# Kernel optimization log

Measured on AMD Instinct MI355X. Metric: run time of the kernel, lower is better.

Reference implementation:

```python
import jax, jax.numpy as jnp
import numpy as np

BH, TQ, TK, DK = 64, 1024, 1024, 64  # B_h = B*H = 4*16


def setup_inputs() -> dict:
    key = jax.random.key(0)
    kq, kk, kv, km = jax.random.split(key, 4)
    Q = jax.random.normal(kq, (BH, TQ, DK), dtype=jnp.float32)
    K = jax.random.normal(kk, (BH, TK, DK), dtype=jnp.float32)
    V = jax.random.normal(kv, (BH, TK, DK), dtype=jnp.float32)
    mask = jax.random.randint(km, (BH, TK), 0, 2).astype(bool)  # 2D padding mask
    return {"Q": Q, "K": K, "V": V, "mask": mask, "head_ablation": 3, "num_heads": 16}


def reference(Q, K, V, mask, head_ablation, num_heads):
    B_h, T_q, d_k = Q.shape
    T_k = K.shape[1]
    # scores = Q K^T / sqrt(d_k), full [B_h, T_q, T_k] matrix as in the original
    scores = jnp.einsum('bqd,bkd->bqk', Q, K) / jnp.sqrt(jnp.asarray(d_k, Q.dtype))
    # 2D mask -> broadcast over query dim (mask.unsqueeze(1).expand in torch)
    m = jnp.broadcast_to(mask[:, None, :], (B_h, T_q, T_k))
    scores = jnp.where(m, scores, jnp.finfo(scores.dtype).min)
    weights = jax.nn.softmax(scores, axis=-1)
    # zero rows whose mask is fully off (torch fully_masked branch)
    fully_masked = m.sum(axis=-1, keepdims=True) == 0
    weights = jnp.where(fully_masked, jnp.zeros((), weights.dtype), weights)
    # head ablation: zero attention weights of one head
    B = B_h // num_heads
    weights = (weights.reshape(B, num_heads, T_q, T_k)
                      .at[:, head_ablation].set(0.0)
                      .reshape(B_h, T_q, T_k))
    # dropout_p = 0.0 -> identity
    output = jnp.einsum('bqk,bkd->bqd', weights, V)
    return (output, weights)
```

## Files before the change

kernel.cpp:

```cpp
#include <hip/hip_runtime.h>
#include <hip/hip_bf16.h>
#include <cfloat>
#include <cstdint>

#define BH 64
#define TQ 1024
#define TK 1024
#define DK 64
#define WSTR 1032

typedef __attribute__((ext_vector_type(8))) short short8;
typedef __attribute__((ext_vector_type(4))) short short4v;
typedef __attribute__((ext_vector_type(4))) float f32x4;

__device__ __forceinline__ short bf16r(float f) {
    union { float f; unsigned u; } x; x.f = f;
    unsigned r = x.u + 0x7fffu + ((x.u >> 16) & 1u);
    return (short)(r >> 16);
}

__device__ __forceinline__ float bf2f(short s) {
    union { unsigned u; float f; } x; x.u = ((unsigned)(unsigned short)s) << 16;
    return x.f;
}

__device__ __forceinline__ short8 load8_bf16_nt(const float* p) {
    f32x4 a = __builtin_nontemporal_load((const f32x4*)p);
    f32x4 b = __builtin_nontemporal_load((const f32x4*)(p + 4));
    short8 r;
    r[0] = bf16r(a[0]); r[1] = bf16r(a[1]); r[2] = bf16r(a[2]); r[3] = bf16r(a[3]);
    r[4] = bf16r(b[0]); r[5] = bf16r(b[1]); r[6] = bf16r(b[2]); r[7] = bf16r(b[3]);
    return r;
}

__device__ __forceinline__ short8 load8_bf16(const float* p) {
    f32x4 a = *(const f32x4*)p;
    f32x4 b = *(const f32x4*)(p + 4);
    short8 r;
    r[0] = bf16r(a[0]); r[1] = bf16r(a[1]); r[2] = bf16r(a[2]); r[3] = bf16r(a[3]);
    r[4] = bf16r(b[0]); r[5] = bf16r(b[1]); r[6] = bf16r(b[2]); r[7] = bf16r(b[3]);
    return r;
}

__global__ __launch_bounds__(256) void pack_kv(const float* __restrict__ K,
                                               const float* __restrict__ V,
                                               const void* __restrict__ mask,
                                               short* __restrict__ Kp,
                                               short* __restrict__ Vp,
                                               float* __restrict__ Mf) {
    __shared__ short tile[64 * 72];
    __shared__ int mflags[2];
    const int tid = threadIdx.x;
    const int bid = blockIdx.x;

    if (bid < 2048) {
        const int g = bid * 256 + tid;
        const int lane = g & 63, half = (g >> 6) & 1, tg = (g >> 7) & 63, b = g >> 13;
        const int key = tg * 16 + (lane & 15);
        const int d = half * 32 + (lane >> 4) * 8;
        short8 o = load8_bf16_nt(K + ((size_t)b * TK + key) * DK + d);
        *(short8*)(Kp + (size_t)g * 8) = o;
    } else if (bid < 3072) {
        const int vb = bid - 2048;
        const int k0 = (vb & 15) * 64, b = vb >> 4;
        #pragma unroll
        for (int it = 0; it < 4; ++it) {
            int lin = it * 256 + tid;
            int kl = lin >> 4;
            int d0 = (lin & 15) * 4;
            f32x4 v = __builtin_nontemporal_load(
                (const f32x4*)(V + ((size_t)b * TK + k0 + kl) * DK + d0));
            short4v o; o[0] = bf16r(v[0]); o[1] = bf16r(v[1]); o[2] = bf16r(v[2]); o[3] = bf16r(v[3]);
            *(short4v*)&tile[kl * 72 + d0] = o;
        }
        __syncthreads();
        #pragma unroll
        for (int it = 0; it < 4; ++it) {
            int lin = it * 256 + tid;
            int d = lin & 63;
            int kg = (lin >> 6) * 4;
            int key = k0 + kg;
            int kk = key >> 5;
            int quad = (kg >> 3) & 3, j0 = kg & 7;
            int lane = (d & 15) + 16 * quad, t = d >> 4;
            short4v o;
            #pragma unroll
            for (int i = 0; i < 4; ++i) o[i] = tile[(kg + i) * 72 + d];
            *(short4v*)&Vp[((((size_t)b * 32 + kk) * 4 + t) * 512) + lane * 8 + j0] = o;
        }
    } else {
        const int b = bid - 3072;
        if (tid == 0) { mflags[0] = 0; mflags[1] = 0; }
        __syncthreads();
        {
            unsigned v = ((const unsigned*)mask)[tid];
            bool f32pat = (v == 0x3f800000u);
            bool u8pat = (v > 1u) && !f32pat;
            unsigned long long bu = __ballot(u8pat);
            unsigned long long bf = __ballot(f32pat);
            if ((tid & 63) == 0) {
                if (bu) atomicOr(&mflags[0], 1);
                if (bf) atomicOr(&mflags[1], 1);
            }
        }
        __syncthreads();
        const int mode = mflags[0] ? 0 : (mflags[1] ? 2 : 1);
        const uint8_t* m8  = (const uint8_t*)mask + (size_t)b * TK;
        const int*     m32 = (const int*)mask     + (size_t)b * TK;
        const float*   mfp = (const float*)mask   + (size_t)b * TK;
        #pragma unroll
        for (int i = 0; i < 4; ++i) {
            int col = i * 256 + tid;
            bool mk = (mode == 0) ? (m8[col] != 0)
                    : (mode == 1) ? (m32[col] != 0)
                                  : (mfp[col] != 0.0f);
            Mf[(size_t)b * TK + col] = mk ? 1.0f : 0.0f;
        }
    }
}

__global__ __launch_bounds__(256, 4) void attn_fused(const float* __restrict__ Q,
                                                     const short* __restrict__ Kp,
                                                     const short* __restrict__ Vp,
                                                     const float* __restrict__ Mf,
                                                     float* __restrict__ Wout,
                                                     float* __restrict__ O,
                                                     const int* __restrict__ ha_p,
                                                     const int* __restrict__ nh_p) {
    __shared__ short Wlds[16 * WSTR];
    __shared__ float red2[16][4];

    const int tid = threadIdx.x;
    const int id = blockIdx.x;
    const int b = (id & 7) + ((id >> 7) & 7) * 8;
    const int qt = (id >> 3) & 15;
    const int q0 = qt * 64;

    if ((b % nh_p[0]) == ha_p[0]) {
        const f32x4 z = {0.f, 0.f, 0.f, 0.f};
        #pragma unroll 4
        for (int i = 0; i < 64; ++i)
            __builtin_nontemporal_store(z, (f32x4*)&Wout[((size_t)b * TQ + q0 + i) * TK + tid * 4]);
        #pragma unroll
        for (int i = 0; i < 4; ++i)
            __builtin_nontemporal_store(z,
                (f32x4*)&O[((size_t)b * TQ + q0 + i * 16 + (tid >> 4)) * DK + (tid & 15) * 4]);
        return;
    }

    const int lane = tid & 63, wave = tid >> 6;
    const int m = lane & 15, quad = lane >> 4;
    const int kw = wave * 256;

    const float* mfp = Mf + (size_t)b * TK + kw;
    const short* kpb = Kp + ((size_t)b * 64 + wave * 16) * 1024 + lane * 8;
    const short* vpb = Vp + (((size_t)b * 32) * 4 + wave) * 512 + lane * 8;

    for (int sub = 0; sub < 4; ++sub) {
        const int qs = q0 + sub * 16;

        const float* qrow = Q + ((size_t)b * TQ + qs + m) * DK + quad * 8;
        short8 a0 = load8_bf16(qrow);
        short8 a1 = load8_bf16(qrow + 32);

        float sum = 0.f;
        #pragma unroll 4
        for (int t = 0; t < 16; ++t) {
            short8 k0 = *(const short8*)(kpb + t * 1024);
            short8 k1 = *(const short8*)(kpb + t * 1024 + 512);
            f32x4 c = {0.f, 0.f, 0.f, 0.f};
            c = __builtin_amdgcn_mfma_f32_16x16x32_bf16(k0, a0, c, 0, 0, 0);
            c = __builtin_amdgcn_mfma_f32_16x16x32_bf16(k1, a1, c, 0, 0, 0);
            float4 mf = *(const float4*)(mfp + t * 16 + quad * 4);
            short4v pw;
            #pragma unroll
            for (int r = 0; r < 4; ++r) {
                float p = ((const float*)&mf)[r] * __expf(fminf(c[r] * 0.125f, 60.f));
                sum += p;
                pw[r] = bf16r(p);
            }
            *(short4v*)&Wlds[m * WSTR + kw + t * 16 + quad * 4] = pw;
        }
        sum += __shfl_xor(sum, 16);
        sum += __shfl_xor(sum, 32);
        if (quad == 0) red2[m][wave] = sum;
        __syncthreads();

        #pragma unroll 4
        for (int i = 0; i < 16; ++i) {
            float4 s4 = *(float4*)red2[i];
            float tot = (s4.x + s4.y) + (s4.z + s4.w);
            float inv = (tot == 0.f) ? 0.f : 1.0f / tot;
            short4v p4 = *(short4v*)&Wlds[i * WSTR + tid * 4];
            f32x4 w;
            w[0] = bf2f(p4[0]) * inv; w[1] = bf2f(p4[1]) * inv;
            w[2] = bf2f(p4[2]) * inv; w[3] = bf2f(p4[3]) * inv;
            __builtin_nontemporal_store(w, (f32x4*)&Wout[((size_t)b * TQ + qs + i) * TK + tid * 4]);
        }

        float inv4[4];
        #pragma unroll
        for (int r = 0; r < 4; ++r) {
            float4 s4 = *(float4*)red2[quad * 4 + r];
            float tot = (s4.x + s4.y) + (s4.z + s4.w);
            inv4[r] = (tot == 0.f) ? 0.f : 1.0f / tot;
        }
        f32x4 oacc = {0.f, 0.f, 0.f, 0.f};
        #pragma unroll 8
        for (int kk = 0; kk < 32; ++kk) {
            short8 a = *(const short8*)&Wlds[m * WSTR + kk * 32 + quad * 8];
            short8 bb = *(const short8*)(vpb + (size_t)kk * 2048);
            oacc = __builtin_amdgcn_mfma_f32_16x16x32_bf16(a, bb, oacc, 0, 0, 0);
        }
        #pragma unroll
        for (int r = 0; r < 4; ++r)
            __builtin_nontemporal_store(oacc[r] * inv4[r],
                &O[((size_t)b * TQ + qs + quad * 4 + r) * DK + wave * 16 + m]);

        __syncthreads();
    }
}

extern "C" void kernel_launch(void* const* d_in, const int* in_sizes, int n_in,
                              void* d_out, int out_size, void* d_ws, size_t ws_size,
                              hipStream_t stream) {
    const float* Q    = (const float*)d_in[0];
    const float* Kmat = (const float*)d_in[1];
    const float* V    = (const float*)d_in[2];
    const void*  mask = d_in[3];
    const int*   ha   = (const int*)d_in[4];
    const int*   nh   = (const int*)d_in[5];

    float* out     = (float*)d_out;
    float* weights = out + (size_t)BH * TQ * DK;

    short* Kp = (short*)d_ws;
    short* Vp = Kp + (size_t)BH * TK * DK;
    float* Mf = (float*)(Vp + (size_t)BH * TK * DK);

    pack_kv<<<dim3(3136), 256, 0, stream>>>(Kmat, V, mask, Kp, Vp, Mf);
    attn_fused<<<dim3(TQ / 64 * BH), 256, 0, stream>>>(Q, Kp, Vp, Mf, weights, out, ha, nh);
}
```

Measured before the change: 357.7 us.

## Fold score scale into K packing, prefetch Q, split PV accumulators

Several micro-optimizations land together. The 1/sqrt(dk) scale is folded into the K bf16 packing, and the fminf clamp is dropped from the exp. The next Q sub-tile is prefetched during the normalization phase. Softmax sums use four independent accumulators, and bf16 packing uses the hardware pair conversion. The PV MFMA chain is split into two accumulators to break the dependency. Dropping the clamp risks overflow if a score exceeds the exp range, and scaling before bf16 rounding slightly changes numerics.

```diff
diff --git a/kernel.cpp b/kernel.cpp
--- a/kernel.cpp
+++ b/kernel.cpp
@@ -24,12 +24,18 @@
     return x.f;
 }
 
-__device__ __forceinline__ short8 load8_bf16_nt(const float* p) {
+__device__ __forceinline__ unsigned pk_bf16(float a, float b) {
+    union { __hip_bfloat162 h; unsigned u; } r;
+    r.h = __float22bfloat162_rn(make_float2(a, b));
+    return r.u;
+}
+
+__device__ __forceinline__ short8 load8_bf16_nt_s(const float* p, float s) {
     f32x4 a = __builtin_nontemporal_load((const f32x4*)p);
     f32x4 b = __builtin_nontemporal_load((const f32x4*)(p + 4));
     short8 r;
-    r[0] = bf16r(a[0]); r[1] = bf16r(a[1]); r[2] = bf16r(a[2]); r[3] = bf16r(a[3]);
-    r[4] = bf16r(b[0]); r[5] = bf16r(b[1]); r[6] = bf16r(b[2]); r[7] = bf16r(b[3]);
+    r[0] = bf16r(a[0] * s); r[1] = bf16r(a[1] * s); r[2] = bf16r(a[2] * s); r[3] = bf16r(a[3] * s);
+    r[4] = bf16r(b[0] * s); r[5] = bf16r(b[1] * s); r[6] = bf16r(b[2] * s); r[7] = bf16r(b[3] * s);
     return r;
 }
 
@@ -58,7 +64,7 @@
         const int lane = g & 63, half = (g >> 6) & 1, tg = (g >> 7) & 63, b = g >> 13;
         const int key = tg * 16 + (lane & 15);
         const int d = half * 32 + (lane >> 4) * 8;
-        short8 o = load8_bf16_nt(K + ((size_t)b * TK + key) * DK + d);
+        short8 o = load8_bf16_nt_s(K + ((size_t)b * TK + key) * DK + d, 0.125f);
         *(short8*)(Kp + (size_t)g * 8) = o;
     } else if (bid < 3072) {
         const int vb = bid - 2048;
@@ -155,15 +161,15 @@
     const float* mfp = Mf + (size_t)b * TK + kw;
     const short* kpb = Kp + ((size_t)b * 64 + wave * 16) * 1024 + lane * 8;
     const short* vpb = Vp + (((size_t)b * 32) * 4 + wave) * 512 + lane * 8;
+    const float* qbase = Q + ((size_t)b * TQ + q0 + m) * DK + quad * 8;
+
+    short8 a0 = load8_bf16(qbase);
+    short8 a1 = load8_bf16(qbase + 32);
 
     for (int sub = 0; sub < 4; ++sub) {
         const int qs = q0 + sub * 16;
 
-        const float* qrow = Q + ((size_t)b * TQ + qs + m) * DK + quad * 8;
-        short8 a0 = load8_bf16(qrow);
-        short8 a1 = load8_bf16(qrow + 32);
-
-        float sum = 0.f;
+        f32x4 sumv = {0.f, 0.f, 0.f, 0.f};
         #pragma unroll 4
         for (int t = 0; t < 16; ++t) {
             short8 k0 = *(const short8*)(kpb + t * 1024);
@@ -172,19 +178,26 @@
             c = __builtin_amdgcn_mfma_f32_16x16x32_bf16(k0, a0, c, 0, 0, 0);
             c = __builtin_amdgcn_mfma_f32_16x16x32_bf16(k1, a1, c, 0, 0, 0);
             float4 mf = *(const float4*)(mfp + t * 16 + quad * 4);
-            short4v pw;
-            #pragma unroll
-            for (int r = 0; r < 4; ++r) {
-                float p = ((const float*)&mf)[r] * __expf(fminf(c[r] * 0.125f, 60.f));
-                sum += p;
-                pw[r] = bf16r(p);
-            }
-            *(short4v*)&Wlds[m * WSTR + kw + t * 16 + quad * 4] = pw;
-        }
+            float p0 = mf.x * __expf(c[0]);
+            float p1 = mf.y * __expf(c[1]);
+            float p2 = mf.z * __expf(c[2]);
+            float p3 = mf.w * __expf(c[3]);
+            sumv[0] += p0; sumv[1] += p1; sumv[2] += p2; sumv[3] += p3;
+            uint2 u2; u2.x = pk_bf16(p0, p1); u2.y = pk_bf16(p2, p3);
+            *(uint2*)&Wlds[m * WSTR + kw + t * 16 + quad * 4] = u2;
+        }
+        float sum = (sumv[0] + sumv[1]) + (sumv[2] + sumv[3]);
         sum += __shfl_xor(sum, 16);
         sum += __shfl_xor(sum, 32);
         if (quad == 0) red2[m][wave] = sum;
         __syncthreads();
+
+        short8 na0, na1;
+        if (sub < 3) {
+            const float* qn = qbase + (size_t)(sub + 1) * 16 * DK;
+            na0 = load8_bf16(qn);
+            na1 = load8_bf16(qn + 32);
+        }
 
         #pragma unroll 4
         for (int i = 0; i < 16; ++i) {
@@ -205,19 +218,24 @@
             float tot = (s4.x + s4.y) + (s4.z + s4.w);
             inv4[r] = (tot == 0.f) ? 0.f : 1.0f / tot;
         }
-        f32x4 oacc = {0.f, 0.f, 0.f, 0.f};
-        #pragma unroll 8
-        for (int kk = 0; kk < 32; ++kk) {
-            short8 a = *(const short8*)&Wlds[m * WSTR + kk * 32 + quad * 8];
-            short8 bb = *(const short8*)(vpb + (size_t)kk * 2048);
-            oacc = __builtin_amdgcn_mfma_f32_16x16x32_bf16(a, bb, oacc, 0, 0, 0);
-        }
+        f32x4 oa = {0.f, 0.f, 0.f, 0.f}, ob = {0.f, 0.f, 0.f, 0.f};
+        #pragma unroll 4
+        for (int kk = 0; kk < 32; kk += 2) {
+            short8 aA = *(const short8*)&Wlds[m * WSTR + kk * 32 + quad * 8];
+            short8 bA = *(const short8*)(vpb + (size_t)kk * 2048);
+            oa = __builtin_amdgcn_mfma_f32_16x16x32_bf16(aA, bA, oa, 0, 0, 0);
+            short8 aB = *(const short8*)&Wlds[m * WSTR + (kk + 1) * 32 + quad * 8];
+            short8 bB = *(const short8*)(vpb + (size_t)(kk + 1) * 2048);
+            ob = __builtin_amdgcn_mfma_f32_16x16x32_bf16(aB, bB, ob, 0, 0, 0);
+        }
+        f32x4 oacc = oa + ob;
         #pragma unroll
         for (int r = 0; r < 4; ++r)
             __builtin_nontemporal_store(oacc[r] * inv4[r],
                 &O[((size_t)b * TQ + qs + quad * 4 + r) * DK + wave * 16 + m]);
 
         __syncthreads();
+        if (sub < 3) { a0 = na0; a1 = na1; }
     }
 }
 
```

Result: no change. 353.7 us (-1.1%).
